# Kernel tuning notes

Hardware: AMD Instinct MI355X
Metric: run time of the kernel (lower is better)

## Reference

```python
import jax, jax.numpy as jnp
import numpy as np

TEMPERATURE = 8.0  # sqrt(d_k=64)

def setup_inputs() -> dict:
    key = jax.random.key(0)
    kq, kk, kv, km1, km2 = jax.random.split(key, 5)
    B, Lq, Lk, D = 128, 512, 512, 64
    q = jax.random.normal(kq, (B, Lq, D), dtype=jnp.float32)
    k = jax.random.normal(kk, (B, Lk, D), dtype=jnp.float32)
    v = jax.random.normal(kv, (B, Lk, D), dtype=jnp.float32)
    key_mask = jax.random.bernoulli(km1, 0.5, (B, Lq, Lk))
    query_mask = jax.random.bernoulli(km2, 0.5, (B, Lq, Lk))
    return {"q": q, "k": k, "v": v, "key_mask": key_mask, "query_mask": query_mask}

def reference(q, k, v, key_mask, query_mask):
    # attn = (q @ k^T) / temperature, pre-softmax key masking with -inf
    scores = jnp.einsum('bqd,bkd->bqk', q, k) / TEMPERATURE
    scores = jnp.where(key_mask, -jnp.inf, scores)
    attn = jax.nn.softmax(scores, axis=-1)
    # post-softmax query-row zeroing
    attn = jnp.where(query_mask, 0.0, attn)
    # dropout omitted (eval mode / deterministic reference)
    output = jnp.einsum('bqk,bkd->bqd', attn, v)
    return (output, attn)
```

## Files before the change

### kernel.cpp

```cpp
#include <hip/hip_runtime.h>
#include <hip/hip_bf16.h>

#define BATCH 128
#define LQ    512
#define LK    512
#define DH    64
#define TQ    16
#define KC    128

#define KSTR  72
#define VROW  136
#define SSTR  520

typedef float    float4v __attribute__((ext_vector_type(4)));
typedef short    short8v __attribute__((ext_vector_type(8)));
typedef short    short4v __attribute__((ext_vector_type(4)));
typedef int      int4v   __attribute__((ext_vector_type(4)));
typedef _Float16 half4v  __attribute__((ext_vector_type(4)));

__device__ __forceinline__ short bf16r(float f) {
  union { float f; unsigned u; } x; x.f = f;
  unsigned r = x.u + 0x7FFFu + ((x.u >> 16) & 1u);
  return (short)(r >> 16);
}

__global__ __launch_bounds__(256, 4)
void sdpa_kernel(const float* __restrict__ Q, const float* __restrict__ K,
                 const float* __restrict__ V, const int* __restrict__ KM,
                 const int* __restrict__ QM, float* __restrict__ OUT,
                 float* __restrict__ ATT)
{
  __shared__ short kvs[KC * KSTR];
  __shared__ short scs[TQ * SSTR];

  const int b    = blockIdx.x >> 5;
  const int q0   = (blockIdx.x & 31) * TQ;
  const int tid  = threadIdx.x;
  const int lane = tid & 63;
  const int wave = tid >> 6;
  const int lm   = lane & 15;
  const int quad = lane >> 4;

  const int row = tid >> 4;
  const int col = tid & 15;
  const size_t gro = (size_t)(b * LQ + q0 + row) * LK;

  int4v kmv[8];
#pragma unroll
  for (int j = 0; j < 8; ++j)
    kmv[j] = *(const int4v*)(KM + gro + col * 4 + j * 64);

  const float* qrow = Q + ((size_t)(b * LQ + q0 + lm)) * DH + quad * 8;
  short8v aq0, aq1;
  {
    float4v f0 = *(const float4v*)(qrow + 0);
    float4v f1 = *(const float4v*)(qrow + 4);
    float4v f2 = *(const float4v*)(qrow + 32);
    float4v f3 = *(const float4v*)(qrow + 36);
#pragma unroll
    for (int e = 0; e < 4; ++e) {
      aq0[e]     = bf16r(f0[e]);
      aq0[e + 4] = bf16r(f1[e]);
      aq1[e]     = bf16r(f2[e]);
      aq1[e + 4] = bf16r(f3[e]);
    }
  }

  for (int kt = 0; kt < LK / KC; ++kt) {
    const float* ksrc = K + ((size_t)(b * LK + kt * KC)) * DH;
#pragma unroll
    for (int i = 0; i < 8; ++i) {
      int fl = (tid + i * 256) << 2;
      int r  = fl >> 6, c = fl & 63;
      float4v d4 = *(const float4v*)(ksrc + fl);
      short4v s4;
      s4[0] = bf16r(d4[0]); s4[1] = bf16r(d4[1]);
      s4[2] = bf16r(d4[2]); s4[3] = bf16r(d4[3]);
      *(short4v*)&kvs[r * KSTR + c] = s4;
    }
    __syncthreads();
#pragma unroll
    for (int t = 0; t < 2; ++t) {
      int ntl = (wave * 2 + t) * 16;
      const short* bp = &kvs[(ntl + lm) * KSTR + quad * 8];
      short8v b0 = *(const short8v*)(bp);
      short8v b1 = *(const short8v*)(bp + 32);
      float4v acc = {0.f, 0.f, 0.f, 0.f};
      acc = __builtin_amdgcn_mfma_f32_16x16x32_bf16(aq0, b0, acc, 0, 0, 0);
      acc = __builtin_amdgcn_mfma_f32_16x16x32_bf16(aq1, b1, acc, 0, 0, 0);
      int n  = kt * KC + ntl + lm;
      int m0 = quad * 4;
#pragma unroll
      for (int j = 0; j < 4; ++j)
        *(_Float16*)&scs[(m0 + j) * SSTR + n] = (_Float16)acc[j];
    }
    __syncthreads();
  }

  float s[32];
  float mx = -INFINITY;
#pragma unroll
  for (int j = 0; j < 8; ++j) {
    half4v h4 = *(const half4v*)&scs[row * SSTR + col * 4 + j * 64];
#pragma unroll
    for (int e = 0; e < 4; ++e) {
      float val = kmv[j][e] ? -INFINITY : (float)h4[e];
      s[j * 4 + e] = val;
      mx = fmaxf(mx, val);
    }
  }
  int4v qmv[8];
#pragma unroll
  for (int j = 0; j < 8; ++j)
    qmv[j] = *(const int4v*)(QM + gro + col * 4 + j * 64);
#pragma unroll
  for (int off = 8; off; off >>= 1) mx = fmaxf(mx, __shfl_xor(mx, off, 64));
  float sum = 0.f;
#pragma unroll
  for (int j = 0; j < 32; ++j) {
    float p = __expf((s[j] - mx) * 0.125f);
    s[j] = p;
    sum += p;
  }
#pragma unroll
  for (int off = 8; off; off >>= 1) sum += __shfl_xor(sum, off, 64);
  const float inv = 1.f / sum;
  float* arow = ATT + gro;
#pragma unroll
  for (int j = 0; j < 8; ++j) {
    int kk = col * 4 + j * 64;
    float4v a4;
#pragma unroll
    for (int e = 0; e < 4; ++e)
      a4[e] = qmv[j][e] ? 0.f : s[j * 4 + e] * inv;
    *(float4v*)(arow + kk) = a4;
    short4v ab;
    ab[0] = bf16r(a4[0]); ab[1] = bf16r(a4[1]);
    ab[2] = bf16r(a4[2]); ab[3] = bf16r(a4[3]);
    *(short4v*)&scs[row * SSTR + kk] = ab;
  }

  float4v oacc = {0.f, 0.f, 0.f, 0.f};
  for (int kt = 0; kt < LK / KC; ++kt) {
    const float* vsrc = V + ((size_t)(b * LK + kt * KC)) * DH;
#pragma unroll
    for (int it = 0; it < 2; ++it) {
      int Bx = tid + 256 * it;
      int bR = Bx >> 4;
      int bC = Bx & 15;
      const float* vp = vsrc + bR * 4 * DH + bC * 4;
      float4v r0 = *(const float4v*)(vp);
      float4v r1 = *(const float4v*)(vp + DH);
      float4v r2 = *(const float4v*)(vp + 2 * DH);
      float4v r3 = *(const float4v*)(vp + 3 * DH);
#pragma unroll
      for (int e = 0; e < 4; ++e) {
        int d  = bC * 4 + e;
        int gp = bR ^ (d & 31);
        short4v s4;
        s4[0] = bf16r(r0[e]); s4[1] = bf16r(r1[e]);
        s4[2] = bf16r(r2[e]); s4[3] = bf16r(r3[e]);
        *(short4v*)&kvs[d * VROW + gp * 4] = s4;
      }
    }
    __syncthreads();
#pragma unroll
    for (int ks = 0; ks < 4; ++ks) {
      const short* ap = &scs[lm * SSTR + kt * KC + ks * 32 + quad * 8];
      short8v a8 = *(const short8v*)ap;
      int n  = wave * 16 + lm;
      int g0 = ks * 8 + quad * 2;
      short4v lo = *(const short4v*)&kvs[n * VROW + ((g0    ) ^ (n & 31)) * 4];
      short4v hi = *(const short4v*)&kvs[n * VROW + ((g0 + 1) ^ (n & 31)) * 4];
      short8v b8;
      b8[0] = lo[0]; b8[1] = lo[1]; b8[2] = lo[2]; b8[3] = lo[3];
      b8[4] = hi[0]; b8[5] = hi[1]; b8[6] = hi[2]; b8[7] = hi[3];
      oacc = __builtin_amdgcn_mfma_f32_16x16x32_bf16(a8, b8, oacc, 0, 0, 0);
    }
    __syncthreads();
  }
  {
    int m0 = quad * 4;
    float* obase = OUT + ((size_t)(b * LQ + q0 + m0)) * DH + wave * 16 + lm;
    obase[0 * DH] = oacc[0];
    obase[1 * DH] = oacc[1];
    obase[2 * DH] = oacc[2];
    obase[3 * DH] = oacc[3];
  }
}

extern "C" void kernel_launch(void* const* d_in, const int* in_sizes, int n_in,
                              void* d_out, int out_size, void* d_ws, size_t ws_size,
                              hipStream_t stream) {
  const float* q  = (const float*)d_in[0];
  const float* k  = (const float*)d_in[1];
  const float* v  = (const float*)d_in[2];
  const int*   km = (const int*)d_in[3];
  const int*   qm = (const int*)d_in[4];
  float* out  = (float*)d_out;
  float* attn = out + (size_t)BATCH * LQ * DH;
  dim3 grid(BATCH * (LQ / TQ));
  dim3 block(256);
  hipLaunchKernelGGL(sdpa_kernel, grid, block, 0, stream,
                     q, k, v, km, qm, out, attn);
}
```

Before: 378.5 us.

## Load K and V fragments directly from global memory, dropping LDS staging

Removes the shared-memory staging buffer for K and V. Each wave now reads its MFMA B-operand fragments straight from global memory and converts them to bf16 in registers, which cuts the per-tile __syncthreads barriers and the LDS footprint. The launch bound is raised to 6 blocks per CU to exploit the lower LDS use, and the key-mask loads are moved after the QK phase to reduce register pressure. In exchange, each K/V element is loaded redundantly by several waves, and the V loads are strided scalar gathers that rely on cache hits instead of coalesced accesses.

```diff
diff --git a/kernel.cpp b/kernel.cpp
--- a/kernel.cpp
+++ b/kernel.cpp
@@ -8,8 +8,6 @@
 #define TQ    16
 #define KC    128
 
-#define KSTR  72
-#define VROW  136
 #define SSTR  520
 
 typedef float    float4v __attribute__((ext_vector_type(4)));
@@ -24,13 +22,12 @@
   return (short)(r >> 16);
 }
 
-__global__ __launch_bounds__(256, 4)
+__global__ __launch_bounds__(256, 6)
 void sdpa_kernel(const float* __restrict__ Q, const float* __restrict__ K,
                  const float* __restrict__ V, const int* __restrict__ KM,
                  const int* __restrict__ QM, float* __restrict__ OUT,
                  float* __restrict__ ATT)
 {
-  __shared__ short kvs[KC * KSTR];
   __shared__ short scs[TQ * SSTR];
 
   const int b    = blockIdx.x >> 5;
@@ -40,15 +37,6 @@
   const int wave = tid >> 6;
   const int lm   = lane & 15;
   const int quad = lane >> 4;
-
-  const int row = tid >> 4;
-  const int col = tid & 15;
-  const size_t gro = (size_t)(b * LQ + q0 + row) * LK;
-
-  int4v kmv[8];
-#pragma unroll
-  for (int j = 0; j < 8; ++j)
-    kmv[j] = *(const int4v*)(KM + gro + col * 4 + j * 64);
 
   const float* qrow = Q + ((size_t)(b * LQ + q0 + lm)) * DH + quad * 8;
   short8v aq0, aq1;
@@ -66,25 +54,25 @@
     }
   }
 
+#pragma unroll
   for (int kt = 0; kt < LK / KC; ++kt) {
-    const float* ksrc = K + ((size_t)(b * LK + kt * KC)) * DH;
-#pragma unroll
-    for (int i = 0; i < 8; ++i) {
-      int fl = (tid + i * 256) << 2;
-      int r  = fl >> 6, c = fl & 63;
-      float4v d4 = *(const float4v*)(ksrc + fl);
-      short4v s4;
-      s4[0] = bf16r(d4[0]); s4[1] = bf16r(d4[1]);
-      s4[2] = bf16r(d4[2]); s4[3] = bf16r(d4[3]);
-      *(short4v*)&kvs[r * KSTR + c] = s4;
-    }
-    __syncthreads();
+    const float* kbase = K + ((size_t)(b * LK + kt * KC)) * DH;
 #pragma unroll
     for (int t = 0; t < 2; ++t) {
       int ntl = (wave * 2 + t) * 16;
-      const short* bp = &kvs[(ntl + lm) * KSTR + quad * 8];
-      short8v b0 = *(const short8v*)(bp);
-      short8v b1 = *(const short8v*)(bp + 32);
+      const float* kr = kbase + (ntl + lm) * DH + quad * 8;
+      float4v f0 = *(const float4v*)(kr + 0);
+      float4v f1 = *(const float4v*)(kr + 4);
+      float4v f2 = *(const float4v*)(kr + 32);
+      float4v f3 = *(const float4v*)(kr + 36);
+      short8v b0, b1;
+#pragma unroll
+      for (int e = 0; e < 4; ++e) {
+        b0[e]     = bf16r(f0[e]);
+        b0[e + 4] = bf16r(f1[e]);
+        b1[e]     = bf16r(f2[e]);
+        b1[e + 4] = bf16r(f3[e]);
+      }
       float4v acc = {0.f, 0.f, 0.f, 0.f};
       acc = __builtin_amdgcn_mfma_f32_16x16x32_bf16(aq0, b0, acc, 0, 0, 0);
       acc = __builtin_amdgcn_mfma_f32_16x16x32_bf16(aq1, b1, acc, 0, 0, 0);
@@ -94,8 +82,19 @@
       for (int j = 0; j < 4; ++j)
         *(_Float16*)&scs[(m0 + j) * SSTR + n] = (_Float16)acc[j];
     }
-    __syncthreads();
   }
+  __syncthreads();
+
+  const int row = tid >> 4;
+  const int col = tid & 15;
+  const size_t gro = (size_t)(b * LQ + q0 + row) * LK;
+  const int* kmr = KM + gro;
+  const int* qmr = QM + gro;
+
+  int4v kmv[8];
+#pragma unroll
+  for (int j = 0; j < 8; ++j)
+    kmv[j] = *(const int4v*)(kmr + col * 4 + j * 64);
 
   float s[32];
   float mx = -INFINITY;
@@ -112,7 +111,7 @@
   int4v qmv[8];
 #pragma unroll
   for (int j = 0; j < 8; ++j)
-    qmv[j] = *(const int4v*)(QM + gro + col * 4 + j * 64);
+    qmv[j] = *(const int4v*)(qmr + col * 4 + j * 64);
 #pragma unroll
   for (int off = 8; off; off >>= 1) mx = fmaxf(mx, __shfl_xor(mx, off, 64));
   float sum = 0.f;
@@ -139,45 +138,22 @@
     ab[2] = bf16r(a4[2]); ab[3] = bf16r(a4[3]);
     *(short4v*)&scs[row * SSTR + kk] = ab;
   }
+  __syncthreads();
 
   float4v oacc = {0.f, 0.f, 0.f, 0.f};
+#pragma unroll
   for (int kt = 0; kt < LK / KC; ++kt) {
-    const float* vsrc = V + ((size_t)(b * LK + kt * KC)) * DH;
-#pragma unroll
-    for (int it = 0; it < 2; ++it) {
-      int Bx = tid + 256 * it;
-      int bR = Bx >> 4;
-      int bC = Bx & 15;
-      const float* vp = vsrc + bR * 4 * DH + bC * 4;
-      float4v r0 = *(const float4v*)(vp);
-      float4v r1 = *(const float4v*)(vp + DH);
-      float4v r2 = *(const float4v*)(vp + 2 * DH);
-      float4v r3 = *(const float4v*)(vp + 3 * DH);
-#pragma unroll
-      for (int e = 0; e < 4; ++e) {
-        int d  = bC * 4 + e;
-        int gp = bR ^ (d & 31);
-        short4v s4;
-        s4[0] = bf16r(r0[e]); s4[1] = bf16r(r1[e]);
-        s4[2] = bf16r(r2[e]); s4[3] = bf16r(r3[e]);
-        *(short4v*)&kvs[d * VROW + gp * 4] = s4;
-      }
-    }
-    __syncthreads();
+    const float* vbase = V + ((size_t)(b * LK + kt * KC)) * DH + wave * 16 + lm;
 #pragma unroll
     for (int ks = 0; ks < 4; ++ks) {
       const short* ap = &scs[lm * SSTR + kt * KC + ks * 32 + quad * 8];
       short8v a8 = *(const short8v*)ap;
-      int n  = wave * 16 + lm;
-      int g0 = ks * 8 + quad * 2;
-      short4v lo = *(const short4v*)&kvs[n * VROW + ((g0    ) ^ (n & 31)) * 4];
-      short4v hi = *(const short4v*)&kvs[n * VROW + ((g0 + 1) ^ (n & 31)) * 4];
       short8v b8;
-      b8[0] = lo[0]; b8[1] = lo[1]; b8[2] = lo[2]; b8[3] = lo[3];
-      b8[4] = hi[0]; b8[5] = hi[1]; b8[6] = hi[2]; b8[7] = hi[3];
+#pragma unroll
+      for (int j = 0; j < 8; ++j)
+        b8[j] = bf16r(vbase[(size_t)(ks * 32 + quad * 8 + j) * DH]);
       oacc = __builtin_amdgcn_mfma_f32_16x16x32_bf16(a8, b8, oacc, 0, 0, 0);
     }
-    __syncthreads();
   }
   {
     int m0 = quad * 4;
```

Result: slower. 422.8 us (+11.7%).

## Load K directly into MFMA registers, prefetch V chunks, add nontemporal accesses

Applied to the files above, without the earlier changes.

QK^T stage now reads K straight from global memory into MFMA operand registers with one-step register prefetch, dropping the K shared-memory staging and its per-chunk barriers. V chunks are prefetched into registers one chunk ahead, and the first chunk is loaded during softmax to overlap global latency. Masks, Q and the attn/output writes use nontemporal loads and stores to reduce cache pollution. This raises register pressure and means each wave fetches K separately, with no reuse through LDS.

```diff
diff --git a/kernel.cpp b/kernel.cpp
--- a/kernel.cpp
+++ b/kernel.cpp
@@ -8,9 +8,8 @@
 #define TQ    16
 #define KC    128
 
-#define KSTR  72
+#define SSTR  520
 #define VROW  136
-#define SSTR  520
 
 typedef float    float4v __attribute__((ext_vector_type(4)));
 typedef short    short8v __attribute__((ext_vector_type(8)));
@@ -22,6 +21,41 @@
   union { float f; unsigned u; } x; x.f = f;
   unsigned r = x.u + 0x7FFFu + ((x.u >> 16) & 1u);
   return (short)(r >> 16);
+}
+
+__device__ __forceinline__ int4v ntload4(const int* p) {
+  return __builtin_nontemporal_load((const int4v*)p);
+}
+
+__device__ __forceinline__ void loadVchunk(const float* __restrict__ vsrc,
+                                           int tid, float4v vr[8]) {
+#pragma unroll
+  for (int it = 0; it < 2; ++it) {
+    int Bx = tid + 256 * it;
+    int bR = Bx >> 4, bC = Bx & 15;
+    const float* vp = vsrc + bR * 4 * DH + bC * 4;
+#pragma unroll
+    for (int r = 0; r < 4; ++r)
+      vr[it * 4 + r] = *(const float4v*)(vp + r * DH);
+  }
+}
+
+__device__ __forceinline__ void storeVchunk(short* vt, int tid,
+                                            const float4v vr[8]) {
+#pragma unroll
+  for (int it = 0; it < 2; ++it) {
+    int Bx = tid + 256 * it;
+    int bR = Bx >> 4, bC = Bx & 15;
+#pragma unroll
+    for (int e = 0; e < 4; ++e) {
+      int d  = bC * 4 + e;
+      int gp = bR ^ (d & 31);
+      short4v s4;
+      s4[0] = bf16r(vr[it * 4 + 0][e]); s4[1] = bf16r(vr[it * 4 + 1][e]);
+      s4[2] = bf16r(vr[it * 4 + 2][e]); s4[3] = bf16r(vr[it * 4 + 3][e]);
+      *(short4v*)&vt[d * VROW + gp * 4] = s4;
+    }
+  }
 }
 
 __global__ __launch_bounds__(256, 4)
@@ -30,8 +64,8 @@
                  const int* __restrict__ QM, float* __restrict__ OUT,
                  float* __restrict__ ATT)
 {
-  __shared__ short kvs[KC * KSTR];
   __shared__ short scs[TQ * SSTR];
+  __shared__ short vt[DH * VROW];
 
   const int b    = blockIdx.x >> 5;
   const int q0   = (blockIdx.x & 31) * TQ;
@@ -48,15 +82,15 @@
   int4v kmv[8];
 #pragma unroll
   for (int j = 0; j < 8; ++j)
-    kmv[j] = *(const int4v*)(KM + gro + col * 4 + j * 64);
+    kmv[j] = ntload4(KM + gro + col * 4 + j * 64);
 
   const float* qrow = Q + ((size_t)(b * LQ + q0 + lm)) * DH + quad * 8;
   short8v aq0, aq1;
   {
-    float4v f0 = *(const float4v*)(qrow + 0);
-    float4v f1 = *(const float4v*)(qrow + 4);
-    float4v f2 = *(const float4v*)(qrow + 32);
-    float4v f3 = *(const float4v*)(qrow + 36);
+    float4v f0 = __builtin_nontemporal_load((const float4v*)(qrow + 0));
+    float4v f1 = __builtin_nontemporal_load((const float4v*)(qrow + 4));
+    float4v f2 = __builtin_nontemporal_load((const float4v*)(qrow + 32));
+    float4v f3 = __builtin_nontemporal_load((const float4v*)(qrow + 36));
 #pragma unroll
     for (int e = 0; e < 4; ++e) {
       aq0[e]     = bf16r(f0[e]);
@@ -66,36 +100,43 @@
     }
   }
 
-  for (int kt = 0; kt < LK / KC; ++kt) {
-    const float* ksrc = K + ((size_t)(b * LK + kt * KC)) * DH;
-#pragma unroll
-    for (int i = 0; i < 8; ++i) {
-      int fl = (tid + i * 256) << 2;
-      int r  = fl >> 6, c = fl & 63;
-      float4v d4 = *(const float4v*)(ksrc + fl);
-      short4v s4;
-      s4[0] = bf16r(d4[0]); s4[1] = bf16r(d4[1]);
-      s4[2] = bf16r(d4[2]); s4[3] = bf16r(d4[3]);
-      *(short4v*)&kvs[r * KSTR + c] = s4;
-    }
-    __syncthreads();
-#pragma unroll
-    for (int t = 0; t < 2; ++t) {
-      int ntl = (wave * 2 + t) * 16;
-      const short* bp = &kvs[(ntl + lm) * KSTR + quad * 8];
-      short8v b0 = *(const short8v*)(bp);
-      short8v b1 = *(const short8v*)(bp + 32);
+  {
+    float4v c0, c1, c2, c3;
+    {
+      const float* kr = K + ((size_t)(b * LK + (wave * 2) * 16 + lm)) * DH + quad * 8;
+      c0 = *(const float4v*)(kr + 0);  c1 = *(const float4v*)(kr + 4);
+      c2 = *(const float4v*)(kr + 32); c3 = *(const float4v*)(kr + 36);
+    }
+#pragma unroll
+    for (int p = 0; p < 8; ++p) {
+      float4v n0, n1, n2, n3;
+      if (p < 7) {
+        int np = p + 1, kt = np >> 1, t = np & 1;
+        const float* kr = K + ((size_t)(b * LK + kt * KC + (wave * 2 + t) * 16 + lm)) * DH + quad * 8;
+        n0 = *(const float4v*)(kr + 0);  n1 = *(const float4v*)(kr + 4);
+        n2 = *(const float4v*)(kr + 32); n3 = *(const float4v*)(kr + 36);
+      }
+      short8v b0, b1;
+#pragma unroll
+      for (int e = 0; e < 4; ++e) {
+        b0[e]     = bf16r(c0[e]);
+        b0[e + 4] = bf16r(c1[e]);
+        b1[e]     = bf16r(c2[e]);
+        b1[e + 4] = bf16r(c3[e]);
+      }
       float4v acc = {0.f, 0.f, 0.f, 0.f};
       acc = __builtin_amdgcn_mfma_f32_16x16x32_bf16(aq0, b0, acc, 0, 0, 0);
       acc = __builtin_amdgcn_mfma_f32_16x16x32_bf16(aq1, b1, acc, 0, 0, 0);
-      int n  = kt * KC + ntl + lm;
+      int kt = p >> 1, t = p & 1;
+      int n  = kt * KC + (wave * 2 + t) * 16 + lm;
       int m0 = quad * 4;
 #pragma unroll
       for (int j = 0; j < 4; ++j)
         *(_Float16*)&scs[(m0 + j) * SSTR + n] = (_Float16)acc[j];
-    }
-    __syncthreads();
-  }
+      if (p < 7) { c0 = n0; c1 = n1; c2 = n2; c3 = n3; }
+    }
+  }
+  __syncthreads();
 
   float s[32];
   float mx = -INFINITY;
@@ -112,7 +153,10 @@
   int4v qmv[8];
 #pragma unroll
   for (int j = 0; j < 8; ++j)
-    qmv[j] = *(const int4v*)(QM + gro + col * 4 + j * 64);
+    qmv[j] = ntload4(QM + gro + col * 4 + j * 64);
+  float4v vr[8];
+  loadVchunk(V + ((size_t)(b * LK)) * DH, tid, vr);
+
 #pragma unroll
   for (int off = 8; off; off >>= 1) mx = fmaxf(mx, __shfl_xor(mx, off, 64));
   float sum = 0.f;
@@ -133,59 +177,45 @@
 #pragma unroll
     for (int e = 0; e < 4; ++e)
       a4[e] = qmv[j][e] ? 0.f : s[j * 4 + e] * inv;
-    *(float4v*)(arow + kk) = a4;
+    __builtin_nontemporal_store(a4, (float4v*)(arow + kk));
     short4v ab;
     ab[0] = bf16r(a4[0]); ab[1] = bf16r(a4[1]);
     ab[2] = bf16r(a4[2]); ab[3] = bf16r(a4[3]);
     *(short4v*)&scs[row * SSTR + kk] = ab;
   }
+  storeVchunk(vt, tid, vr);
+  __syncthreads();
 
   float4v oacc = {0.f, 0.f, 0.f, 0.f};
-  for (int kt = 0; kt < LK / KC; ++kt) {
-    const float* vsrc = V + ((size_t)(b * LK + kt * KC)) * DH;
-#pragma unroll
-    for (int it = 0; it < 2; ++it) {
-      int Bx = tid + 256 * it;
-      int bR = Bx >> 4;
-      int bC = Bx & 15;
-      const float* vp = vsrc + bR * 4 * DH + bC * 4;
-      float4v r0 = *(const float4v*)(vp);
-      float4v r1 = *(const float4v*)(vp + DH);
-      float4v r2 = *(const float4v*)(vp + 2 * DH);
-      float4v r3 = *(const float4v*)(vp + 3 * DH);
-#pragma unroll
-      for (int e = 0; e < 4; ++e) {
-        int d  = bC * 4 + e;
-        int gp = bR ^ (d & 31);
-        short4v s4;
-        s4[0] = bf16r(r0[e]); s4[1] = bf16r(r1[e]);
-        s4[2] = bf16r(r2[e]); s4[3] = bf16r(r3[e]);
-        *(short4v*)&kvs[d * VROW + gp * 4] = s4;
-      }
-    }
-    __syncthreads();
+#pragma unroll
+  for (int kt = 0; kt < 4; ++kt) {
+    if (kt < 3)
+      loadVchunk(V + ((size_t)(b * LK + (kt + 1) * KC)) * DH, tid, vr);
 #pragma unroll
     for (int ks = 0; ks < 4; ++ks) {
       const short* ap = &scs[lm * SSTR + kt * KC + ks * 32 + quad * 8];
       short8v a8 = *(const short8v*)ap;
       int n  = wave * 16 + lm;
       int g0 = ks * 8 + quad * 2;
-      short4v lo = *(const short4v*)&kvs[n * VROW + ((g0    ) ^ (n & 31)) * 4];
-      short4v hi = *(const short4v*)&kvs[n * VROW + ((g0 + 1) ^ (n & 31)) * 4];
+      short4v lo = *(const short4v*)&vt[n * VROW + ((g0    ) ^ (n & 31)) * 4];
+      short4v hi = *(const short4v*)&vt[n * VROW + ((g0 + 1) ^ (n & 31)) * 4];
       short8v b8;
       b8[0] = lo[0]; b8[1] = lo[1]; b8[2] = lo[2]; b8[3] = lo[3];
       b8[4] = hi[0]; b8[5] = hi[1]; b8[6] = hi[2]; b8[7] = hi[3];
       oacc = __builtin_amdgcn_mfma_f32_16x16x32_bf16(a8, b8, oacc, 0, 0, 0);
     }
-    __syncthreads();
+    if (kt < 3) {
+      __syncthreads();
+      storeVchunk(vt, tid, vr);
+      __syncthreads();
+    }
   }
   {
     int m0 = quad * 4;
     float* obase = OUT + ((size_t)(b * LQ + q0 + m0)) * DH + wave * 16 + lm;
-    obase[0 * DH] = oacc[0];
-    obase[1 * DH] = oacc[1];
-    obase[2 * DH] = oacc[2];
-    obase[3 * DH] = oacc[3];
+#pragma unroll
+    for (int j = 0; j < 4; ++j)
+      __builtin_nontemporal_store(oacc[j], obase + j * DH);
   }
 }
 
```

New measurement: 388.4 us. +2.6%, slower.
